# Kernel tuning notes

Hardware: AMD Instinct MI355X
Metric: run time of the kernel (lower is better)

The kernel has to match this reference:

```python
import jax, jax.numpy as jnp
import numpy as np

BN_EPS = 1e-5
SG = jax.lax.stop_gradient


def _silu(z):
    return z * jax.nn.sigmoid(z)


def _binary_activation(x):
    # forward value = sign(x); backward goes through piecewise quadratic out3 (STE)
    out1 = jnp.where(x < -1, -1.0, x * x + 2 * x)
    out2 = jnp.where(x < 0, out1, -x * x + 2 * x)
    out3 = jnp.where(x < 1, out2, 1.0)
    return SG(jnp.sign(x)) - SG(out3) + out3


def _binarize_weight(w):
    # per-output-channel scaling factor * sign(w), STE through clipped weights
    sf = SG(jnp.mean(jnp.abs(w), axis=(1, 2, 3), keepdims=True))  # [O,1,1,1]
    cw = jnp.clip(w, -1.0, 1.0)
    return SG(sf * jnp.sign(w)) - SG(cw) + cw


def _conv3x3_s2(x, w, b):
    y = jax.lax.conv_general_dilated(
        x, w, window_strides=(2, 2), padding=((1, 1), (1, 1)),
        dimension_numbers=("NCHW", "OIHW", "NCHW"))
    return y + b[None, :, None, None]


def _batchnorm_train(x, gamma, beta):
    # training-mode BN: batch statistics over (N,H,W), biased variance
    mean = jnp.mean(x, axis=(0, 2, 3), keepdims=True)
    var = jnp.mean((x - mean) ** 2, axis=(0, 2, 3), keepdims=True)
    xhat = (x - mean) * jax.lax.rsqrt(var + BN_EPS)
    return xhat * gamma[None, :, None, None] + beta[None, :, None, None]


def _learnable_bias(x, emb, w, b):
    # bias = zero_module(linear)(SiLU(emb)) broadcast over H,W
    bias = _silu(emb) @ w.T + b  # [B, C]
    return x + bias[:, :, None, None]


def _avgpool2(x):
    B, C, H, W = x.shape
    return x.reshape(B, C, H // 2, 2, W // 2, 2).mean(axis=(3, 5))


def setup_inputs() -> dict:
    key = jax.random.key(0)
    ks = jax.random.split(key, 16)
    B, Cin, P, E, H, W = 32, 128, 256, 512, 64, 64
    scalor = P // Cin  # 2
    inp = {
        "x": jax.random.normal(ks[0], (B, Cin, H, W), jnp.float32),
        "emb": jax.random.normal(ks[1], (B, E), jnp.float32),
        "m1_w": jax.random.normal(ks[2], (Cin, E), jnp.float32) * 0.02,
        "m1_b": jnp.zeros((Cin,), jnp.float32),
        "conv_w": jax.random.uniform(ks[3], (scalor, Cin, Cin, 3, 3), jnp.float32, -1.0, 1.0) * 0.1,
        "conv_b": jax.random.normal(ks[4], (scalor, Cin), jnp.float32) * 0.01,
        "bn_g": jnp.ones((scalor, Cin), jnp.float32),
        "bn_b": jnp.zeros((scalor, Cin), jnp.float32),
        "m2_w": jax.random.normal(ks[5], (P, E), jnp.float32) * 0.02,
        "m2_b": jnp.zeros((P,), jnp.float32),
        "prelu_a": jnp.full((P,), 0.25, jnp.float32),
        "m3_w": jax.random.normal(ks[6], (P, E), jnp.float32) * 0.02,
        "m3_b": jnp.zeros((P,), jnp.float32),
    }
    return inp


def reference(x, emb, m1_w, m1_b, conv_w, conv_b, bn_g, bn_b,
              m2_w, m2_b, prelu_a, m3_w, m3_b):
    scalor = conv_w.shape[0]
    out = _learnable_bias(x, emb, m1_w, m1_b)
    out = _binary_activation(out)
    xp = _avgpool2(x)  # residual, [B,Cin,H/2,W/2]
    out_list = []
    for i in range(scalor):
        bw = _binarize_weight(conv_w[i])
        y = _conv3x3_s2(out, bw, conv_b[i])
        y = _batchnorm_train(y, bn_g[i], bn_b[i])
        out_list.append(y + xp)
    o = jnp.concatenate(out_list, axis=1)  # [B, planes, H/2, W/2]
    o = _learnable_bias(o, emb, m2_w, m2_b)
    a = prelu_a[None, :, None, None]
    o = jnp.where(o > 0, o, a * o)  # PReLU per channel
    o = _learnable_bias(o, emb, m3_w, m3_b)
    return o
```

## Files before the change

kernel.cpp:

```cpp
#include <hip/hip_runtime.h>
#include <cstdint>
#include <cstddef>

#define B_  32
#define CIN 128
#define P_  256
#define E_  512
#define H_  64
#define W_  64
#define HO  32
#define WO  32

#define APITCH 65
#define APIX   4225

__global__ void k_bw(const float* __restrict__ emb,
                     const float* __restrict__ m1_w, const float* __restrict__ m1_b,
                     const float* __restrict__ m2_w, const float* __restrict__ m2_b,
                     const float* __restrict__ m3_w, const float* __restrict__ m3_b,
                     const float* __restrict__ conv_w,
                     float* __restrict__ b1, float* __restrict__ b2, float* __restrict__ b3,
                     float* __restrict__ sf, unsigned int* __restrict__ wbits,
                     int* __restrict__ cwrow, int* __restrict__ cwcol, int* __restrict__ cw0,
                     float* __restrict__ s1, float* __restrict__ s2) {
    int bid = blockIdx.x;
    int tid = threadIdx.x;
    int wave = tid >> 6, lane = tid & 63;

    if (bid < B_ * 160) {
        int n = bid / 160, rg = bid % 160;
        int row = rg * 4 + wave;
        const float* sp = emb + n * E_;
        const float* wrow; float bias; float* dst;
        if (row < CIN)            { wrow = m1_w + (size_t)row * E_;          bias = m1_b[row]; dst = b1 + n * CIN + row; }
        else if (row < CIN + P_)  { int c = row - CIN;      wrow = m2_w + (size_t)c * E_; bias = m2_b[c]; dst = b2 + n * P_ + c; }
        else                      { int c = row - CIN - P_; wrow = m3_w + (size_t)c * E_; bias = m3_b[c]; dst = b3 + n * P_ + c; }
        float acc = 0.f;
        #pragma unroll
        for (int j = 0; j < 8; j++) {
            int k = j * 64 + lane;
            float e = sp[k];
            acc += (e / (1.f + expf(-e))) * wrow[k];
        }
        #pragma unroll
        for (int off = 32; off > 0; off >>= 1) acc += __shfl_down(acc, off);
        if (lane == 0) *dst = acc + bias;
        return;
    }

    int base = (bid - B_ * 160) * 2;
    int oc = base + (wave >> 1);
    int iw = wave & 1;
    int i  = iw * 64 + lane;
    if (lane == 0 && iw == 0) { s1[oc] = 0.f; s2[oc] = 0.f; }
    const float* wp = conv_w + ((size_t)oc * CIN + i) * 9;
    float w[9]; float s = 0.f;
    int pc[9];
    #pragma unroll
    for (int t = 0; t < 9; t++) { w[t] = wp[t]; s += fabsf(w[t]); }
    #pragma unroll
    for (int t = 0; t < 9; t++) {
        unsigned long long m = __ballot(w[t] < 0.f);
        pc[t] = __popcll(m);
        if (lane == 0) {
            wbits[oc * 36 + t * 4 + iw * 2 + 0] = (unsigned int)(m & 0xffffffffull);
            wbits[oc * 36 + t * 4 + iw * 2 + 1] = (unsigned int)(m >> 32);
        }
    }
    #pragma unroll
    for (int off = 32; off > 0; off >>= 1) s += __shfl_down(s, off);
    __shared__ float sred[4];
    __shared__ int spc[4][9];
    if (lane == 0) {
        sred[wave] = s;
        #pragma unroll
        for (int t = 0; t < 9; t++) spc[wave][t] = pc[t];
    }
    __syncthreads();
    if (tid == 0) {
        sf[base] = (sred[0] + sred[1]) / 1152.f;
        int c_[9];
        #pragma unroll
        for (int t = 0; t < 9; t++) c_[t] = spc[0][t] + spc[1][t];
        cwrow[base] = 384 - 2 * (c_[0] + c_[1] + c_[2]);
        cwcol[base] = 384 - 2 * (c_[0] + c_[3] + c_[6]);
        cw0[base]   = 128 - 2 * c_[0];
    } else if (tid == 128) {
        sf[base + 1] = (sred[2] + sred[3]) / 1152.f;
        int c_[9];
        #pragma unroll
        for (int t = 0; t < 9; t++) c_[t] = spc[2][t] + spc[3][t];
        cwrow[base + 1] = 384 - 2 * (c_[0] + c_[1] + c_[2]);
        cwcol[base + 1] = 384 - 2 * (c_[0] + c_[3] + c_[6]);
        cw0[base + 1]   = 128 - 2 * c_[0];
    }
}

__global__ void k_prep(const float* __restrict__ x, const float* __restrict__ b1,
                       unsigned int* __restrict__ abits, float* __restrict__ xpool) {
    __shared__ float sb1[CIN];
    int n = blockIdx.x >> 5, h2 = blockIdx.x & 31;
    int tid = threadIdx.x;
    for (int i = tid; i < CIN; i += 256) sb1[i] = b1[n * CIN + i];
    __syncthreads();

    if (h2 == 0) {
        for (int i = tid; i < 129; i += 256) {
            size_t idx = (i < 65) ? ((size_t)n * APIX + i)
                                  : ((size_t)n * APIX + (size_t)(i - 64) * APITCH);
            ((uint4*)abits)[idx] = make_uint4(0u, 0u, 0u, 0u);
        }
    }

    int pix = tid >> 1, half = tid & 1;
    int h = 2 * h2 + (pix >> 6), w = pix & 63;
    const float* xp = x + ((size_t)n * CIN + half * 64) * (H_ * W_) + (size_t)h * W_ + w;
    unsigned int wds[2];
    #pragma unroll
    for (int wd = 0; wd < 2; wd++) {
        unsigned int m = 0;
        #pragma unroll
        for (int b = 0; b < 32; b++) {
            float v = xp[(size_t)(wd * 32 + b) * (H_ * W_)] + sb1[half * 64 + wd * 32 + b];
            m |= (v < 0.f ? 1u : 0u) << b;
        }
        wds[wd] = m;
    }
    ((uint2*)abits)[((size_t)n * APIX + (size_t)(h + 1) * APITCH + (w + 1)) * 2 + half] =
        make_uint2(wds[0], wds[1]);

    for (int idx = tid; idx < CIN * WO; idx += 256) {
        int c = idx >> 5, w2 = idx & 31;
        const float* p = x + ((size_t)n * CIN + c) * (H_ * W_) + (size_t)(2 * h2) * W_ + 2 * w2;
        float2 a = *(const float2*)p;
        float2 b = *(const float2*)(p + W_);
        xpool[((size_t)n * CIN + c) * (HO * WO) + h2 * WO + w2] = 0.25f * (a.x + a.y + b.x + b.y);
    }
}

__global__ void __launch_bounds__(256, 6) k_convstat(const unsigned int* __restrict__ abits,
                                                     const unsigned int* __restrict__ wbits,
                                                     const int* __restrict__ cwrow,
                                                     const int* __restrict__ cwcol,
                                                     const int* __restrict__ cw0,
                                                     short* __restrict__ y16,
                                                     float* __restrict__ s1, float* __restrict__ s2) {
    __shared__ int red1[16][33], red2[16][33];
    int bid = blockIdx.x;
    int strip = bid & 3, og = (bid >> 2) & 15, n = bid >> 6;
    int tid = threadIdx.x;
    int wave = tid >> 6, lane = tid & 63;
    int oh = strip * 8 + (tid >> 5), ow = tid & 31;
    bool r0 = (oh == 0), c0 = (ow == 0);
    bool rc0 = r0 && c0;

    const uint4* asrc = ((const uint4*)abits) + (size_t)n * APIX;
    uint4 img[9];
    #pragma unroll
    for (int kh = 0; kh < 3; kh++) {
        #pragma unroll
        for (int kw = 0; kw < 3; kw++) {
            img[kh * 3 + kw] = asrc[(2 * oh + kh) * APITCH + (2 * ow + kw)];
        }
    }

    int ocb = og * 16;
    const uint4* wp = ((const uint4*)wbits) + (size_t)ocb * 9;
    short* yp = y16 + (((size_t)n * P_ + ocb) << 10) + strip * 256 + tid;
    #pragma unroll 4
    for (int o = 0; o < 16; o++) {
        int popsum = 0;
        #pragma unroll
        for (int t = 0; t < 9; t++) {
            uint4 a = img[t];
            uint4 w = wp[o * 9 + t];
            popsum += __popc(a.x ^ w.x) + __popc(a.y ^ w.y) +
                      __popc(a.z ^ w.z) + __popc(a.w ^ w.w);
        }
        int srow = cwrow[ocb + o], scol = cwcol[ocb + o], sz = cw0[ocb + o];
        int corr = (r0 ? srow : 0) + (c0 ? scol : 0) - (rc0 ? sz : 0);
        int s = 1152 - 2 * popsum - corr;
        yp[(size_t)o << 10] = (short)s;
        int vs = s, v2 = s * s;
        vs += __shfl_down(vs, 32); v2 += __shfl_down(v2, 32);
        vs += __shfl_down(vs, 16); v2 += __shfl_down(v2, 16);
        vs += __shfl_down(vs, 8);  v2 += __shfl_down(v2, 8);
        if (lane < 8) { red1[o][wave * 8 + lane] = vs; red2[o][wave * 8 + lane] = v2; }
    }
    __syncthreads();
    if (tid < 32) {
        int o = tid & 15;
        int a = 0;
        if (tid < 16) {
            #pragma unroll
            for (int p = 0; p < 32; p++) a += red1[o][p];
            atomicAdd(s1 + ocb + o, (float)a);
        } else {
            #pragma unroll
            for (int p = 0; p < 32; p++) a += red2[o][p];
            atomicAdd(s2 + ocb + o, (float)a);
        }
    }
}

__global__ void k_epi(const short* __restrict__ y16, const float* __restrict__ xpool,
                      const float* __restrict__ sf,
                      const float* __restrict__ s1, const float* __restrict__ s2,
                      const float* __restrict__ bn_g, const float* __restrict__ bn_b,
                      const float* __restrict__ b2, const float* __restrict__ b3,
                      const float* __restrict__ prelu_a, float* __restrict__ out) {
    int i4 = blockIdx.x * blockDim.x + threadIdx.x;
    int pix4 = i4 & 255;
    int c = (i4 >> 8) & 255;
    int n = i4 >> 16;
    short4 yv = ((const short4*)y16)[i4];
    float4 xv = ((const float4*)xpool)[((n * CIN + (c & 127)) << 8) + pix4];
    const float inv = 1.f / (B_ * HO * WO);
    float sc = sf[c];
    float m = sc * s1[c] * inv;
    float var = fmaf(-m, m, sc * sc * s2[c] * inv);
    float r = rsqrtf(var + 1e-5f) * bn_g[c];
    float add0 = bn_b[c] + b2[n * P_ + c];
    float a = prelu_a[c];
    float b3v = b3[n * P_ + c];
    float o0 = (sc * (float)yv.x - m) * r + add0 + xv.x; o0 = (o0 > 0.f ? o0 : a * o0) + b3v;
    float o1 = (sc * (float)yv.y - m) * r + add0 + xv.y; o1 = (o1 > 0.f ? o1 : a * o1) + b3v;
    float o2 = (sc * (float)yv.z - m) * r + add0 + xv.z; o2 = (o2 > 0.f ? o2 : a * o2) + b3v;
    float o3 = (sc * (float)yv.w - m) * r + add0 + xv.w; o3 = (o3 > 0.f ? o3 : a * o3) + b3v;
    ((float4*)out)[i4] = make_float4(o0, o1, o2, o3);
}

extern "C" void kernel_launch(void* const* d_in, const int* in_sizes, int n_in,
                              void* d_out, int out_size, void* d_ws, size_t ws_size,
                              hipStream_t stream) {
    const float* x      = (const float*)d_in[0];
    const float* emb    = (const float*)d_in[1];
    const float* m1_w   = (const float*)d_in[2];
    const float* m1_b   = (const float*)d_in[3];
    const float* conv_w = (const float*)d_in[4];
    const float* bn_g   = (const float*)d_in[6];
    const float* bn_b   = (const float*)d_in[7];
    const float* m2_w   = (const float*)d_in[8];
    const float* m2_b   = (const float*)d_in[9];
    const float* prelu_a= (const float*)d_in[10];
    const float* m3_w   = (const float*)d_in[11];
    const float* m3_b   = (const float*)d_in[12];

    float* out = (float*)d_out;

    float* wsf = (float*)d_ws;
    float* b1    = wsf;
    float* b2    = wsf + 4096;
    float* b3    = wsf + 12288;
    float* sf    = wsf + 20480;
    float* s1    = wsf + 20736;
    float* s2    = wsf + 20992;
    unsigned int* wbits = (unsigned int*)(wsf + 21248);
    int* cwrow = (int*)(wsf + 30464);
    int* cwcol = (int*)(wsf + 30720);
    int* cw0   = (int*)(wsf + 30976);
    unsigned int* abits = (unsigned int*)(wsf + 31232);
    float* xpool = wsf + 572032;
    short* y16   = (short*)(wsf + 4766336);

    k_bw      <<<B_ * 160 + P_ / 2, 256, 0, stream>>>(emb, m1_w, m1_b, m2_w, m2_b, m3_w, m3_b,
                                                      conv_w, b1, b2, b3, sf, wbits,
                                                      cwrow, cwcol, cw0, s1, s2);
    k_prep    <<<B_ * 32, 256, 0, stream>>>(x, b1, abits, xpool);
    k_convstat<<<B_ * 64, 256, 0, stream>>>(abits, wbits, cwrow, cwcol, cw0, y16, s1, s2);
    k_epi     <<<(B_ * P_ * HO * WO) / (4 * 256), 256, 0, stream>>>(y16, xpool, sf, s1, s2,
                                                                    bn_g, bn_b, b2, b3, prelu_a, out);
}
```

Before: 186.9 us.

## Restructure prep loads, split BN stats out of conv into separate kernel

```diff
diff --git a/kernel.cpp b/kernel.cpp
--- a/kernel.cpp
+++ b/kernel.cpp
@@ -112,44 +112,36 @@
         }
     }
 
-    int pix = tid >> 1, half = tid & 1;
-    int h = 2 * h2 + (pix >> 6), w = pix & 63;
-    const float* xp = x + ((size_t)n * CIN + half * 64) * (H_ * W_) + (size_t)h * W_ + w;
-    unsigned int wds[2];
-    #pragma unroll
-    for (int wd = 0; wd < 2; wd++) {
-        unsigned int m = 0;
-        #pragma unroll
-        for (int b = 0; b < 32; b++) {
-            float v = xp[(size_t)(wd * 32 + b) * (H_ * W_)] + sb1[half * 64 + wd * 32 + b];
-            m |= (v < 0.f ? 1u : 0u) << b;
-        }
-        wds[wd] = m;
-    }
-    ((uint2*)abits)[((size_t)n * APIX + (size_t)(h + 1) * APITCH + (w + 1)) * 2 + half] =
-        make_uint2(wds[0], wds[1]);
-
-    for (int idx = tid; idx < CIN * WO; idx += 256) {
-        int c = idx >> 5, w2 = idx & 31;
-        const float* p = x + ((size_t)n * CIN + c) * (H_ * W_) + (size_t)(2 * h2) * W_ + 2 * w2;
-        float2 a = *(const float2*)p;
-        float2 b = *(const float2*)(p + W_);
-        xpool[((size_t)n * CIN + c) * (HO * WO) + h2 * WO + w2] = 0.25f * (a.x + a.y + b.x + b.y);
-    }
-}
-
-__global__ void __launch_bounds__(256, 6) k_convstat(const unsigned int* __restrict__ abits,
-                                                     const unsigned int* __restrict__ wbits,
-                                                     const int* __restrict__ cwrow,
-                                                     const int* __restrict__ cwcol,
-                                                     const int* __restrict__ cw0,
-                                                     short* __restrict__ y16,
-                                                     float* __restrict__ s1, float* __restrict__ s2) {
-    __shared__ int red1[16][33], red2[16][33];
+    int wg = tid >> 6, lane = tid & 63;
+    int w = lane, w2 = w >> 1;
+    const float* xb = x + ((size_t)(n * CIN + wg * 32)) * (H_ * W_) + (size_t)(2 * h2) * W_ + w;
+    float* xpq = xpool + ((size_t)(n * CIN + wg * 32)) * (HO * WO) + h2 * WO + w2;
+    unsigned int mt = 0, mb = 0;
+    #pragma unroll 8
+    for (int j = 0; j < 32; j++) {
+        float vt = xb[(size_t)j * (H_ * W_)];
+        float vb = xb[(size_t)j * (H_ * W_) + W_];
+        float bc = sb1[wg * 32 + j];
+        mt |= (vt + bc < 0.f ? 1u : 0u) << j;
+        mb |= (vb + bc < 0.f ? 1u : 0u) << j;
+        float p = vt + vb;
+        p += __shfl_xor(p, 1);
+        if ((w & 1) == 0) xpq[(size_t)j * (HO * WO)] = 0.25f * p;
+    }
+    size_t basei = ((size_t)n * APIX + (size_t)(2 * h2 + 1) * APITCH + (w + 1)) * 4 + wg;
+    abits[basei] = mt;
+    abits[basei + APITCH * 4] = mb;
+}
+
+__global__ void __launch_bounds__(256, 8) k_conv(const unsigned int* __restrict__ abits,
+                                                 const unsigned int* __restrict__ wbits,
+                                                 const int* __restrict__ cwrow,
+                                                 const int* __restrict__ cwcol,
+                                                 const int* __restrict__ cw0,
+                                                 short* __restrict__ y16) {
     int bid = blockIdx.x;
     int strip = bid & 3, og = (bid >> 2) & 15, n = bid >> 6;
     int tid = threadIdx.x;
-    int wave = tid >> 6, lane = tid & 63;
     int oh = strip * 8 + (tid >> 5), ow = tid & 31;
     bool r0 = (oh == 0), c0 = (ow == 0);
     bool rc0 = r0 && c0;
@@ -166,41 +158,50 @@
 
     int ocb = og * 16;
     const uint4* wp = ((const uint4*)wbits) + (size_t)ocb * 9;
+    int popsum[16];
+    #pragma unroll
+    for (int o = 0; o < 16; o++) popsum[o] = 0;
+    #pragma unroll
+    for (int t = 0; t < 9; t++) {
+        uint4 a = img[t];
+        #pragma unroll
+        for (int o = 0; o < 16; o++) {
+            uint4 w = wp[o * 9 + t];
+            popsum[o] += __popc(a.x ^ w.x) + __popc(a.y ^ w.y) +
+                         __popc(a.z ^ w.z) + __popc(a.w ^ w.w);
+        }
+    }
     short* yp = y16 + (((size_t)n * P_ + ocb) << 10) + strip * 256 + tid;
-    #pragma unroll 4
+    #pragma unroll
     for (int o = 0; o < 16; o++) {
-        int popsum = 0;
-        #pragma unroll
-        for (int t = 0; t < 9; t++) {
-            uint4 a = img[t];
-            uint4 w = wp[o * 9 + t];
-            popsum += __popc(a.x ^ w.x) + __popc(a.y ^ w.y) +
-                      __popc(a.z ^ w.z) + __popc(a.w ^ w.w);
-        }
-        int srow = cwrow[ocb + o], scol = cwcol[ocb + o], sz = cw0[ocb + o];
-        int corr = (r0 ? srow : 0) + (c0 ? scol : 0) - (rc0 ? sz : 0);
-        int s = 1152 - 2 * popsum - corr;
+        int corr = (r0 ? cwrow[ocb + o] : 0) + (c0 ? cwcol[ocb + o] : 0) - (rc0 ? cw0[ocb + o] : 0);
+        int s = 1152 - 2 * popsum[o] - corr;
         yp[(size_t)o << 10] = (short)s;
-        int vs = s, v2 = s * s;
-        vs += __shfl_down(vs, 32); v2 += __shfl_down(v2, 32);
-        vs += __shfl_down(vs, 16); v2 += __shfl_down(v2, 16);
-        vs += __shfl_down(vs, 8);  v2 += __shfl_down(v2, 8);
-        if (lane < 8) { red1[o][wave * 8 + lane] = vs; red2[o][wave * 8 + lane] = v2; }
-    }
+    }
+}
+
+__global__ void k_stat(const short* __restrict__ y16,
+                       float* __restrict__ s1, float* __restrict__ s2) {
+    int oc = blockIdx.x & 255, nq = blockIdx.x >> 8;
+    int tid = threadIdx.x;
+    int acc = 0, acc2 = 0;
+    #pragma unroll
+    for (int k = 0; k < 8; k++) {
+        int n = nq * 8 + k;
+        short4 v = ((const short4*)(y16 + (((size_t)n * P_ + oc) << 10)))[tid];
+        int a0 = v.x, a1 = v.y, a2 = v.z, a3 = v.w;
+        acc  += a0 + a1 + a2 + a3;
+        acc2 += a0 * a0 + a1 * a1 + a2 * a2 + a3 * a3;
+    }
+    float f1 = (float)acc, f2 = (float)acc2;
+    #pragma unroll
+    for (int off = 32; off > 0; off >>= 1) { f1 += __shfl_down(f1, off); f2 += __shfl_down(f2, off); }
+    __shared__ float r1[4], r2[4];
+    int wave = tid >> 6, lane = tid & 63;
+    if (lane == 0) { r1[wave] = f1; r2[wave] = f2; }
     __syncthreads();
-    if (tid < 32) {
-        int o = tid & 15;
-        int a = 0;
-        if (tid < 16) {
-            #pragma unroll
-            for (int p = 0; p < 32; p++) a += red1[o][p];
-            atomicAdd(s1 + ocb + o, (float)a);
-        } else {
-            #pragma unroll
-            for (int p = 0; p < 32; p++) a += red2[o][p];
-            atomicAdd(s2 + ocb + o, (float)a);
-        }
-    }
+    if (tid == 0)       atomicAdd(s1 + oc, r1[0] + r1[1] + r1[2] + r1[3]);
+    else if (tid == 64) atomicAdd(s2 + oc, r2[0] + r2[1] + r2[2] + r2[3]);
 }
 
 __global__ void k_epi(const short* __restrict__ y16, const float* __restrict__ xpool,
@@ -263,11 +264,12 @@
     float* xpool = wsf + 572032;
     short* y16   = (short*)(wsf + 4766336);
 
-    k_bw      <<<B_ * 160 + P_ / 2, 256, 0, stream>>>(emb, m1_w, m1_b, m2_w, m2_b, m3_w, m3_b,
-                                                      conv_w, b1, b2, b3, sf, wbits,
-                                                      cwrow, cwcol, cw0, s1, s2);
-    k_prep    <<<B_ * 32, 256, 0, stream>>>(x, b1, abits, xpool);
-    k_convstat<<<B_ * 64, 256, 0, stream>>>(abits, wbits, cwrow, cwcol, cw0, y16, s1, s2);
-    k_epi     <<<(B_ * P_ * HO * WO) / (4 * 256), 256, 0, stream>>>(y16, xpool, sf, s1, s2,
-                                                                    bn_g, bn_b, b2, b3, prelu_a, out);
-}
+    k_bw   <<<B_ * 160 + P_ / 2, 256, 0, stream>>>(emb, m1_w, m1_b, m2_w, m2_b, m3_w, m3_b,
+                                                   conv_w, b1, b2, b3, sf, wbits,
+                                                   cwrow, cwcol, cw0, s1, s2);
+    k_prep <<<B_ * 32, 256, 0, stream>>>(x, b1, abits, xpool);
+    k_conv <<<B_ * 64, 256, 0, stream>>>(abits, wbits, cwrow, cwcol, cw0, y16);
+    k_stat <<<4 * P_, 256, 0, stream>>>(y16, s1, s2);
+    k_epi  <<<(B_ * P_ * HO * WO) / (4 * 256), 256, 0, stream>>>(y16, xpool, sf, s1, s2,
+                                                                 bn_g, bn_b, b2, b3, prelu_a, out);
+}
```

Result: slower. 206.5 us (+10.5%).

## Fuse sign-bit packing with avgpool in prep and pin image bits in registers

Applied to the files above, without the earlier changes.

```diff
diff --git a/kernel.cpp b/kernel.cpp
--- a/kernel.cpp
+++ b/kernel.cpp
@@ -112,30 +112,26 @@
         }
     }
 
-    int pix = tid >> 1, half = tid & 1;
-    int h = 2 * h2 + (pix >> 6), w = pix & 63;
-    const float* xp = x + ((size_t)n * CIN + half * 64) * (H_ * W_) + (size_t)h * W_ + w;
-    unsigned int wds[2];
-    #pragma unroll
-    for (int wd = 0; wd < 2; wd++) {
-        unsigned int m = 0;
-        #pragma unroll
-        for (int b = 0; b < 32; b++) {
-            float v = xp[(size_t)(wd * 32 + b) * (H_ * W_)] + sb1[half * 64 + wd * 32 + b];
-            m |= (v < 0.f ? 1u : 0u) << b;
-        }
-        wds[wd] = m;
-    }
-    ((uint2*)abits)[((size_t)n * APIX + (size_t)(h + 1) * APITCH + (w + 1)) * 2 + half] =
-        make_uint2(wds[0], wds[1]);
-
-    for (int idx = tid; idx < CIN * WO; idx += 256) {
-        int c = idx >> 5, w2 = idx & 31;
-        const float* p = x + ((size_t)n * CIN + c) * (H_ * W_) + (size_t)(2 * h2) * W_ + 2 * w2;
-        float2 a = *(const float2*)p;
-        float2 b = *(const float2*)(p + W_);
-        xpool[((size_t)n * CIN + c) * (HO * WO) + h2 * WO + w2] = 0.25f * (a.x + a.y + b.x + b.y);
-    }
+    int wg = tid >> 6, lane = tid & 63;
+    int row = lane >> 5;
+    int wp2 = lane & 31;
+    int h = 2 * h2 + row;
+    const float* xb = x + ((size_t)(n * CIN + wg * 32)) * (H_ * W_) + (size_t)h * W_ + 2 * wp2;
+    float* xpq = xpool + ((size_t)(n * CIN + wg * 32)) * (HO * WO) + h2 * WO + wp2;
+    unsigned int m0 = 0, m1 = 0;
+    #pragma unroll 8
+    for (int j = 0; j < 32; j++) {
+        float2 v = *(const float2*)(xb + (size_t)j * (H_ * W_));
+        float bc = sb1[wg * 32 + j];
+        m0 |= (v.x + bc < 0.f ? 1u : 0u) << j;
+        m1 |= (v.y + bc < 0.f ? 1u : 0u) << j;
+        float p = v.x + v.y;
+        p += __shfl_xor(p, 32);
+        if (row == 0) xpq[(size_t)j * (HO * WO)] = 0.25f * p;
+    }
+    size_t basei = ((size_t)n * APIX + (size_t)(h + 1) * APITCH + (2 * wp2 + 1)) * 4 + wg;
+    abits[basei]     = m0;
+    abits[basei + 4] = m1;
 }
 
 __global__ void __launch_bounds__(256, 6) k_convstat(const unsigned int* __restrict__ abits,
@@ -163,6 +159,10 @@
             img[kh * 3 + kw] = asrc[(2 * oh + kh) * APITCH + (2 * ow + kw)];
         }
     }
+    #pragma unroll
+    for (int t = 0; t < 9; t++) {
+        asm volatile("" : "+v"(img[t].x), "+v"(img[t].y), "+v"(img[t].z), "+v"(img[t].w));
+    }
 
     int ocb = og * 16;
     const uint4* wp = ((const uint4*)wbits) + (size_t)ocb * 9;
@@ -177,8 +177,7 @@
             popsum += __popc(a.x ^ w.x) + __popc(a.y ^ w.y) +
                       __popc(a.z ^ w.z) + __popc(a.w ^ w.w);
         }
-        int srow = cwrow[ocb + o], scol = cwcol[ocb + o], sz = cw0[ocb + o];
-        int corr = (r0 ? srow : 0) + (c0 ? scol : 0) - (rc0 ? sz : 0);
+        int corr = (r0 ? cwrow[ocb + o] : 0) + (c0 ? cwcol[ocb + o] : 0) - (rc0 ? cw0[ocb + o] : 0);
         int s = 1152 - 2 * popsum - corr;
         yp[(size_t)o << 10] = (short)s;
         int vs = s, v2 = s * s;
```

Measured after the change: 186.2 us. Within noise of the previous version (-0.4%).
